# Kernel optimization log

Hardware: AMD Instinct MI355X
Metric: run time of the kernel (lower is better)

The kernel has to match this reference:

```python
import jax, jax.numpy as jnp
import numpy as np

B, S, SE = 4, 1024, 1024
E, H, M = 768, 12, 100
D = E // H
EPS = 1e-5
GELU_C = 0.7978845608028654  # sqrt(2/pi)


def _ln(x, g, b):
    mu = x.mean(-1, keepdims=True)
    v = ((x - mu) ** 2).mean(-1, keepdims=True)
    return g * (x - mu) / jnp.sqrt(v + EPS) + b


def _gelu(x):
    return 0.5 * x * (1.0 + jnp.tanh(GELU_C * (x + 0.044715 * x ** 3)))


def _split(x):  # [b,s,E] -> [b,H,s,D]
    b, s, _ = x.shape
    return x.reshape(b, s, H, D).transpose(0, 2, 1, 3)


def _merge(x):  # [b,H,s,D] -> [b,s,E]
    b, h, s, d = x.shape
    return x.transpose(0, 2, 1, 3).reshape(b, s, h * d)


def _forward(x, encoder_features, ln1_g, ln1_b, ln2_g, ln2_b,
             c_attn_w, c_attn_b, attn_proj_w, attn_proj_b,
             memory_features, mem_attn_w, mem_attn_b, mem_alpha_w, mem_alpha_b,
             fcq_w, fcq_b, fck_w, fck_b, fcv_w, fcv_b, enc_proj_w, enc_proj_b,
             fc_alpha1_w, fc_alpha1_b, fc_alpha2_w, fc_alpha2_b,
             mlp_fc_w, mlp_fc_b, mlp_proj_w, mlp_proj_b, mask_encoder):
    # ---- memory-augmented self-attention (note: original has NO 1/sqrt(d) scaling here) ----
    h = _ln(x, ln1_g, ln1_b)
    qkv = h @ c_attn_w + c_attn_b
    q, k, v = jnp.split(qkv, 3, axis=-1)
    q, k, v = _split(q), _split(k), _split(v)
    w = jax.nn.softmax(jnp.einsum('bhqd,bhkd->bhqk', q, k), axis=-1)
    a = _merge(jnp.einsum('bhqk,bhkd->bhqd', w, v))
    # memory slots are batch-independent -> compute once, broadcast over batch
    mem = memory_features[0] @ mem_attn_w + mem_attn_b  # [M, 2E]
    mk, mv = jnp.split(mem, 2, axis=-1)
    mk = mk.reshape(M, H, D).transpose(1, 2, 0)  # [H,D,M]
    mv = mv.reshape(M, H, D).transpose(1, 0, 2)  # [H,M,D]
    wm = jax.nn.softmax(jnp.einsum('bhqd,hdm->bhqm', q, mk), axis=-1)
    a1 = _merge(jnp.einsum('bhqm,hmd->bhqd', wm, mv))
    al = jax.nn.sigmoid(jnp.concatenate([a, a1], -1) @ mem_alpha_w + mem_alpha_b)
    a = al * a + (1.0 - al) * a1
    a = a @ attn_proj_w + attn_proj_b
    a = x + a  # residual (dropout = identity in eval)

    # ---- two cross-attentions sharing weights and ln_1 ----
    ha = _ln(a, ln1_g, ln1_b)

    def enc_dec(enc):
        qe = _split(ha @ fcq_w + fcq_b)
        ke = _split(enc @ fck_w + fck_b)
        ve = _split(enc @ fcv_w + fcv_b)
        we = jnp.einsum('bhqd,bhkd->bhqk', qe, ke) / np.float32(np.sqrt(D))
        we = jnp.where(mask_encoder, jnp.float32(-10000.0), we)
        we = jax.nn.softmax(we, axis=-1)
        o = _merge(jnp.einsum('bhqk,bhkd->bhqd', we, ve))
        return o @ enc_proj_w + enc_proj_b

    e1 = enc_dec(_ln(encoder_features[:, 0], ln1_g, ln1_b))
    e2 = enc_dec(_ln(encoder_features[:, 1], ln1_g, ln1_b))
    al1 = jax.nn.sigmoid(jnp.concatenate([a, e1], -1) @ fc_alpha1_w + fc_alpha1_b)
    al2 = jax.nn.sigmoid(jnp.concatenate([a, e2], -1) @ fc_alpha2_w + fc_alpha2_b)
    e1 = al1 * a + (1.0 - al1) * e1
    e2 = al2 * a + (1.0 - al2) * e2
    a = (e1 + e2) / np.float32(np.sqrt(2.0))

    # ---- MLP ----
    hm = _ln(a, ln2_g, ln2_b)
    m = _gelu(hm @ mlp_fc_w + mlp_fc_b) @ mlp_proj_w + mlp_proj_b
    return a + m


def setup_inputs() -> dict:
    key = jax.random.key(0)
    ks = iter(jax.random.split(key, 48))

    def rn(shape, s=0.02):
        return jax.random.normal(next(ks), shape, jnp.float32) * s

    return dict(
        x=jax.random.normal(next(ks), (B, S, E), jnp.float32),
        encoder_features=jax.random.normal(next(ks), (B, 2, SE, E), jnp.float32),
        mask_encoder=jax.random.bernoulli(next(ks), 0.1, (B, 1, 1, SE)),
        ln1_g=jnp.ones(E, jnp.float32), ln1_b=jnp.zeros(E, jnp.float32),
        ln2_g=jnp.ones(E, jnp.float32), ln2_b=jnp.zeros(E, jnp.float32),
        c_attn_w=rn((E, 3 * E)), c_attn_b=jnp.zeros(3 * E, jnp.float32),
        attn_proj_w=rn((E, E)), attn_proj_b=jnp.zeros(E, jnp.float32),
        memory_features=rn((1, M, E), 1.0),
        mem_attn_w=rn((E, 2 * E)), mem_attn_b=jnp.zeros(2 * E, jnp.float32),
        mem_alpha_w=rn((2 * E, E)), mem_alpha_b=jnp.zeros(E, jnp.float32),
        fcq_w=rn((E, E)), fcq_b=jnp.zeros(E, jnp.float32),
        fck_w=rn((E, E)), fck_b=jnp.zeros(E, jnp.float32),
        fcv_w=rn((E, E)), fcv_b=jnp.zeros(E, jnp.float32),
        enc_proj_w=rn((E, E)), enc_proj_b=jnp.zeros(E, jnp.float32),
        fc_alpha1_w=rn((2 * E, E)), fc_alpha1_b=jnp.zeros(E, jnp.float32),
        fc_alpha2_w=rn((2 * E, E)), fc_alpha2_b=jnp.zeros(E, jnp.float32),
        mlp_fc_w=rn((E, 4 * E)), mlp_fc_b=jnp.zeros(4 * E, jnp.float32),
        mlp_proj_w=rn((4 * E, E)), mlp_proj_b=jnp.zeros(E, jnp.float32),
    )


def reference(x, encoder_features, mask_encoder, ln1_g, ln1_b, ln2_g, ln2_b,
              c_attn_w, c_attn_b, attn_proj_w, attn_proj_b,
              memory_features, mem_attn_w, mem_attn_b, mem_alpha_w, mem_alpha_b,
              fcq_w, fcq_b, fck_w, fck_b, fcv_w, fcv_b, enc_proj_w, enc_proj_b,
              fc_alpha1_w, fc_alpha1_b, fc_alpha2_w, fc_alpha2_b,
              mlp_fc_w, mlp_fc_b, mlp_proj_w, mlp_proj_b):
    return _forward(x, encoder_features, ln1_g, ln1_b, ln2_g, ln2_b,
                    c_attn_w, c_attn_b, attn_proj_w, attn_proj_b,
                    memory_features, mem_attn_w, mem_attn_b, mem_alpha_w, mem_alpha_b,
                    fcq_w, fcq_b, fck_w, fck_b, fcv_w, fcv_b, enc_proj_w, enc_proj_b,
                    fc_alpha1_w, fc_alpha1_b, fc_alpha2_w, fc_alpha2_b,
                    mlp_fc_w, mlp_fc_b, mlp_proj_w, mlp_proj_b, mask_encoder)
```

## Files before the change

### kernel.cpp

```cpp
#include <hip/hip_runtime.h>

typedef __bf16 bf16_t;
typedef __bf16 bf16x8v __attribute__((ext_vector_type(8)));
typedef float f32x4 __attribute__((ext_vector_type(4)));

#define CB 4
#define CE 768
#define CH 12
#define CD 64

__device__ __forceinline__ float fexp2(float x) { return __builtin_amdgcn_exp2f(x); }

__device__ __forceinline__ void gload16(const void* g, void* l) {
    __builtin_amdgcn_global_load_lds((const __attribute__((address_space(1))) void*)g,
                                     (__attribute__((address_space(3))) void*)l, 16, 0, 0);
}

__device__ __forceinline__ void xcd_remap(int& bx, int& by, int gx, int gy) {
    int nwg = gx * gy;
    if ((nwg & 7) == 0) {
        int lin = by * gx + bx;
        int lin2 = (lin & 7) * (nwg >> 3) + (lin >> 3);
        bx = lin2 % gx;
        by = lin2 / gx;
    }
}

template<int BM, int BN, int CONCAT, int ACT, int RES, int OUT, int CMODE>
__global__ __launch_bounds__(256)
void gemm_n(const bf16_t* __restrict__ A0, const bf16_t* __restrict__ A1,
            const bf16_t* __restrict__ Bt, const float* __restrict__ bias,
            const float* __restrict__ bias2, const void* __restrict__ resid,
            void* __restrict__ C, void* __restrict__ C2, void* __restrict__ C3,
            int M, int N, int K, int lda, int ldc)
{
    constexpr int WM = BM / 2, WN = BN / 2, RM = WM / 16, RN = WN / 16;
    __shared__ __align__(16) bf16_t As0[BM * 64], As1[BM * 64];
    __shared__ __align__(16) bf16_t Bs0[BN * 64], Bs1[BN * 64];

    const int t = threadIdx.x;
    const int lane = t & 63, wave = t >> 6;
    int bx = blockIdx.x, by = blockIdx.y;
    xcd_remap(bx, by, gridDim.x, gridDim.y);
    const int m0 = by * BM, n0 = bx * BN;
    const int wm = (wave & 1) * WM, wn = (wave >> 1) * WN;
    const int fr = lane & 15, quad = lane >> 4;

    const int lr = lane >> 3;
    const int kof = ((lane & 7) ^ lr) * 8;

    const bf16_t* A1b = A1;
    if (CMODE == 6) A1b = A1 + (n0 >= 768 ? (long)4096 * 768 : 0);

    f32x4 acc[RM][RN];
#pragma unroll
    for (int i = 0; i < RM; i++)
#pragma unroll
        for (int j = 0; j < RN; j++)
#pragma unroll
            for (int p = 0; p < 4; p++) acc[i][j][p] = 0.f;

    auto stage = [&](bf16_t* As, bf16_t* Bs, int kt) {
        const bf16_t* Ab = A0;
        int kk = kt;
        if (CONCAT && kt >= 768) { Ab = A1b; kk = kt - 768; }
        const bf16_t* asrc = Ab + (long)(m0 + wave * 8 + lr) * lda + kk + kof;
#pragma unroll
        for (int c = 0; c < BM / 32; ++c)
            gload16(asrc + (long)c * 32 * lda, &As[(c * 32 + wave * 8) * 64]);
        const bf16_t* bsrc = Bt + (long)(n0 + wave * 8 + lr) * K + kt + kof;
#pragma unroll
        for (int c = 0; c < BN / 32; ++c)
            gload16(bsrc + (long)c * 32 * K, &Bs[(c * 32 + wave * 8) * 64]);
    };

    const int sw = fr & 7;
    auto compute = [&](const bf16_t* As, const bf16_t* Bs) {
        bf16x8v af[RM][2], bfr[RN][2];
        const int s0 = quad ^ sw;
#pragma unroll
        for (int i = 0; i < RM; ++i) {
            const char* rb = (const char*)As + (wm + i * 16 + fr) * 128;
            af[i][0] = *(const bf16x8v*)(rb + (s0 << 4));
            af[i][1] = *(const bf16x8v*)(rb + ((s0 ^ 4) << 4));
        }
#pragma unroll
        for (int j = 0; j < RN; ++j) {
            const char* rb = (const char*)Bs + (wn + j * 16 + fr) * 128;
            bfr[j][0] = *(const bf16x8v*)(rb + (s0 << 4));
            bfr[j][1] = *(const bf16x8v*)(rb + ((s0 ^ 4) << 4));
        }
#pragma unroll
        for (int ks = 0; ks < 2; ++ks)
#pragma unroll
            for (int i = 0; i < RM; ++i)
#pragma unroll
                for (int j = 0; j < RN; ++j)
                    acc[i][j] = __builtin_amdgcn_mfma_f32_16x16x32_bf16(af[i][ks], bfr[j][ks], acc[i][j], 0, 0, 0);
    };

    const int nk = K >> 6;
    stage(As0, Bs0, 0);
    __syncthreads();
    for (int kt = 0; kt + 2 <= nk; kt += 2) {
        stage(As1, Bs1, (kt + 1) << 6);
        compute(As0, Bs0);
        __syncthreads();
        if (kt + 2 < nk) stage(As0, Bs0, (kt + 2) << 6);
        compute(As1, Bs1);
        __syncthreads();
    }

    const int rq = quad * 4, cn = fr;
#pragma unroll
    for (int i = 0; i < RM; i++)
#pragma unroll
        for (int j = 0; j < RN; j++) {
            int col = n0 + wn + j * 16 + cn;
            int t3 = (CMODE == 4 || CMODE == 5) ? (col / 768) : 0;
            int cc = col - t3 * 768;
            float bv = 0.f;
            if (CMODE == 5)      bv = t3 ? bias2[cc] : bias[cc];
            else if (CMODE == 6) bv = (col < 768) ? bias[col] : bias2[col - 768];
            else if (bias)       bv = bias[col];
            const int row0 = m0 + wm + i * 16 + rq;
            float vv[4];
#pragma unroll
            for (int p = 0; p < 4; p++) {
                float v = acc[i][j][p] + bv;
                if (ACT == 1) v = 1.f / (1.f + __expf(-v));
                if (ACT == 2) {
                    float u2 = 1.5957691216057308f * (v + 0.044715f * v * v * v);
                    v = v / (1.f + __expf(-u2));
                }
                if (RES == 2) v += ((const float*)resid)[(long)(row0 + p) * ldc + col];
                vv[p] = v;
            }
            if (CMODE == 0) {
#pragma unroll
                for (int p = 0; p < 4; p++) {
                    long idx = (long)(row0 + p) * ldc + col;
                    if (OUT == 0)      ((bf16_t*)C)[idx] = (bf16_t)vv[p];
                    else if (OUT == 1) ((float*)C)[idx] = vv[p];
                    else { ((float*)C)[idx] = vv[p]; ((bf16_t*)C2)[idx] = (bf16_t)vv[p]; }
                }
            } else if (CMODE == 6) {
                long base = (col < 768) ? 0 : ((long)4096 * 768 - 768);
#pragma unroll
                for (int p = 0; p < 4; p++)
                    ((bf16_t*)C)[base + (long)(row0 + p) * 768 + col] = (bf16_t)vv[p];
            } else if (CMODE == 7) {
#pragma unroll
                for (int p = 0; p < 4; p++) {
                    long idx = (long)(row0 + p) * ldc + col;
                    float a  = (float)((const bf16_t*)C2)[idx];
                    float a1 = (float)((const bf16_t*)C3)[idx];
                    ((bf16_t*)C)[idx] = (bf16_t)(vv[p] * a + (1.f - vv[p]) * a1);
                }
            } else {
                int bb = row0 >> 10, ss0 = row0 & 1023;
                int hh = cc >> 6, dd = cc & 63;
                long srow = (long)(bb * CH + hh) * 1024 + ss0;
                long tbase = (((long)(bb * CH + hh) * 64) + dd) * 1024 + ss0;
                union { ushort4 u4; bf16_t b[4]; } pk;
#pragma unroll
                for (int p = 0; p < 4; p++) pk.b[p] = (bf16_t)vv[p];
                if (CMODE == 2) {
#pragma unroll
                    for (int p = 0; p < 4; p++)
                        ((bf16_t*)C)[(srow + p) * 64 + dd] = pk.b[p];
                } else if (CMODE == 5) {
                    if (t3 == 0) {
#pragma unroll
                        for (int p = 0; p < 4; p++)
                            ((bf16_t*)C)[(srow + p) * 64 + dd] = pk.b[p];
                    } else {
                        *(ushort4*)((bf16_t*)C2 + tbase) = pk.u4;
                    }
                } else {
                    if (t3 == 0) {
#pragma unroll
                        for (int p = 0; p < 4; p++)
                            ((bf16_t*)C)[(srow + p) * 64 + dd] = pk.b[p];
                    } else if (t3 == 1) {
#pragma unroll
                        for (int p = 0; p < 4; p++)
                            ((bf16_t*)C2)[(srow + p) * 64 + dd] = pk.b[p];
                    } else {
                        *(ushort4*)((bf16_t*)C3 + tbase) = pk.u4;
                    }
                }
            }
        }
}

template<int MODE, int QR>
__global__ __launch_bounds__(256)
void flash_attn(const bf16_t* __restrict__ Q, const bf16_t* __restrict__ K,
                const bf16_t* __restrict__ V, const int* __restrict__ mask,
                bf16_t* __restrict__ O)
{
    constexpr int QG = QR / 64;
    __shared__ __align__(16) bf16_t Qs[QR * 64];
    __shared__ __align__(16) bf16_t Ks0[64 * 64], Ks1[64 * 64];
    __shared__ __align__(16) bf16_t Vs[64 * 64];

    const int t = threadIdx.x;
    const int lane = t & 63, wave = t >> 6;
    int bx = blockIdx.x, bz = blockIdx.z;
    {
        int nwg = gridDim.x * gridDim.z;
        if ((nwg & 7) == 0) {
            int lin = bz * gridDim.x + bx;
            int lin2 = (lin & 7) * (nwg >> 3) + (lin >> 3);
            bx = lin2 % gridDim.x;
            bz = lin2 / gridDim.x;
        }
    }
    const int zq = (MODE == 1) ? (bz % 48) : bz;
    const int b = zq / CH, h = bz % CH;
    const long eoff = (MODE == 1) ? (long)(bz / 48) * ((long)4096 * 768) : 0;
    const int q0 = bx * QR;

    const bf16_t* Qb = Q + (long)zq * 65536 + (long)q0 * 64;
    const bf16_t* Kb = (MODE == 2) ? K + (long)h * (128 * 64) : K + (long)bz * 65536;
    const bf16_t* Vb = (MODE == 2) ? V + (long)h * (64 * 128) : V + (long)bz * 65536;
    const int ldv = (MODE == 2) ? 128 : 1024;
    const int NT = (MODE == 2) ? 2 : 16;
    constexpr float SCL = (MODE == 1) ? 0.18033688011112042f : 1.4426950408889634f;

    const int lr = lane >> 3, kof = ((lane & 7) ^ lr) * 8;

    auto stageK = [&](bf16_t* Ks, int kt) {
#pragma unroll
        for (int c = 0; c < 2; ++c) {
            int r = wave * 8 + c * 32;
            gload16(Kb + (long)(kt * 64 + r + lr) * 64 + kof, &Ks[r * 64]);
        }
    };
    auto stageV = [&](int kt) {
#pragma unroll
        for (int c = 0; c < 2; ++c) {
            int r = wave * 8 + c * 32;
            gload16(Vb + (long)(r + lr) * ldv + kt * 64 + kof, &Vs[r * 64]);
        }
    };

    stageK(Ks0, 0);
#pragma unroll
    for (int c = 0; c < QR / 32; ++c) {
        int r = wave * 8 + c * 32;
        gload16(Qb + (long)(r + lr) * 64 + kof, &Qs[r * 64]);
    }
    __syncthreads();

    const int fr = lane & 15, quad = lane >> 4;
    const int sw = fr & 7;
    bf16x8v qf[QG][2];
#pragma unroll
    for (int g = 0; g < QG; g++)
#pragma unroll
        for (int ks = 0; ks < 2; ks++) {
            const char* rb = (const char*)Qs + (wave * (16 * QG) + g * 16 + fr) * 128;
            bf16x8v raw = *(const bf16x8v*)(rb + (((quad ^ sw) ^ (ks << 2)) << 4));
#pragma unroll
            for (int i = 0; i < 8; i++) qf[g][ks][i] = (bf16_t)((float)raw[i] * SCL);
        }

    bf16_t* Ps = &Qs[wave * (16 * QG) * 64];

    f32x4 o[4][QG];
    float mrow[QG], lrow[QG];
#pragma unroll
    for (int g = 0; g < QG; g++) { mrow[g] = -1e30f; lrow[g] = 0.f; }
#pragma unroll
    for (int j = 0; j < 4; j++)
#pragma unroll
        for (int g = 0; g < QG; g++)
#pragma unroll
            for (int p = 0; p < 4; p++) o[j][g][p] = 0.f;

    auto qkt_sm = [&](const bf16_t* Ks, int kt) {
        f32x4 s[4][QG];
#pragma unroll
        for (int j = 0; j < 4; j++)
#pragma unroll
            for (int g = 0; g < QG; g++)
#pragma unroll
                for (int p = 0; p < 4; p++) s[j][g][p] = 0.f;
        __builtin_amdgcn_s_setprio(1);
#pragma unroll
        for (int ks = 0; ks < 2; ks++) {
            bf16x8v bk[4];
#pragma unroll
            for (int j = 0; j < 4; j++) {
                const char* rb = (const char*)Ks + (j * 16 + fr) * 128;
                bk[j] = *(const bf16x8v*)(rb + (((quad ^ sw) ^ (ks << 2)) << 4));
            }
#pragma unroll
            for (int j = 0; j < 4; j++)
#pragma unroll
                for (int g = 0; g < QG; g++)
                    s[j][g] = __builtin_amdgcn_mfma_f32_16x16x32_bf16(bk[j], qf[g][ks], s[j][g], 0, 0, 0);
        }
        __builtin_amdgcn_s_setprio(0);
        if (MODE == 1) {
#pragma unroll
            for (int j = 0; j < 4; j++) {
                int4 mv = *(const int4*)&mask[(long)b * 1024 + kt * 64 + j * 16 + quad * 4];
#pragma unroll
                for (int g = 0; g < QG; g++) {
                    s[j][g][0] = mv.x ? -14426.95f : s[j][g][0];
                    s[j][g][1] = mv.y ? -14426.95f : s[j][g][1];
                    s[j][g][2] = mv.z ? -14426.95f : s[j][g][2];
                    s[j][g][3] = mv.w ? -14426.95f : s[j][g][3];
                }
            }
        }
        if (MODE == 2) {
#pragma unroll
            for (int j = 0; j < 4; j++)
#pragma unroll
                for (int p = 0; p < 4; p++)
                    if (kt * 64 + j * 16 + quad * 4 + p >= 100)
#pragma unroll
                        for (int g = 0; g < QG; g++) s[j][g][p] = -1e30f;
        }
        float tmax[QG];
        bool need = false;
#pragma unroll
        for (int g = 0; g < QG; g++) {
            float tm = s[0][g][0];
#pragma unroll
            for (int j = 0; j < 4; j++)
#pragma unroll
                for (int p = 0; p < 4; p++) tm = fmaxf(tm, s[j][g][p]);
            tm = fmaxf(tm, __shfl_xor(tm, 16, 64));
            tm = fmaxf(tm, __shfl_xor(tm, 32, 64));
            tmax[g] = tm;
            need = need || (tm > mrow[g] + 8.f);
        }
        if (__any(need ? 1 : 0)) {
#pragma unroll
            for (int g = 0; g < QG; g++) {
                float mnew = fmaxf(mrow[g], tmax[g]);
                float alpha = fexp2(mrow[g] - mnew);
                lrow[g] *= alpha;
                mrow[g] = mnew;
                float arow[4];
#pragma unroll
                for (int p = 0; p < 4; p++)
                    arow[p] = __shfl(alpha, (lane & 48) | (quad * 4 + p), 64);
#pragma unroll
                for (int j = 0; j < 4; j++)
#pragma unroll
                    for (int p = 0; p < 4; p++) o[j][g][p] *= arow[p];
            }
        }
#pragma unroll
        for (int g = 0; g < QG; g++) {
            float rs = 0.f;
#pragma unroll
            for (int j = 0; j < 4; j++)
#pragma unroll
                for (int p = 0; p < 4; p++) {
                    float e = fexp2(s[j][g][p] - mrow[g]);
                    s[j][g][p] = e;
                    rs += e;
                }
            rs += __shfl_xor(rs, 16, 64);
            rs += __shfl_xor(rs, 32, 64);
            lrow[g] += rs;
        }
#pragma unroll
        for (int j = 0; j < 4; j++)
#pragma unroll
            for (int g = 0; g < QG; g++) {
                union { uint2 u; bf16_t bb[4]; } pk;
#pragma unroll
                for (int p = 0; p < 4; p++) pk.bb[p] = (bf16_t)s[j][g][p];
                int row = g * 16 + fr;
                *(uint2*)((char*)Ps + row * 128 +
                          (((j * 2 + (quad >> 1)) ^ sw) << 4) + ((quad & 1) << 3)) = pk.u;
            }
    };

    auto pv = [&]() {
        __builtin_amdgcn_s_setprio(1);
#pragma unroll
        for (int ks = 0; ks < 2; ks++) {
            bf16x8v af[QG], bv[4];
#pragma unroll
            for (int g = 0; g < QG; g++) {
                const char* rb = (const char*)Ps + (g * 16 + fr) * 128;
                af[g] = *(const bf16x8v*)(rb + (((quad ^ sw) ^ (ks << 2)) << 4));
            }
#pragma unroll
            for (int j = 0; j < 4; j++) {
                const char* rb = (const char*)Vs + (j * 16 + fr) * 128;
                bv[j] = *(const bf16x8v*)(rb + (((quad ^ sw) ^ (ks << 2)) << 4));
            }
#pragma unroll
            for (int j = 0; j < 4; j++)
#pragma unroll
                for (int g = 0; g < QG; g++)
                    o[j][g] = __builtin_amdgcn_mfma_f32_16x16x32_bf16(af[g], bv[j], o[j][g], 0, 0, 0);
        }
        __builtin_amdgcn_s_setprio(0);
    };

    for (int kt = 0; kt < NT; kt += 2) {
        stageV(kt);
        if (kt + 1 < NT) stageK(Ks1, kt + 1);
        qkt_sm(Ks0, kt);
        __syncthreads();
        pv();
        __syncthreads();
        stageV(kt + 1);
        if (kt + 2 < NT) stageK(Ks0, kt + 2);
        qkt_sm(Ks1, kt + 1);
        __syncthreads();
        pv();
        __syncthreads();
    }
#pragma unroll
    for (int g = 0; g < QG; g++) {
        float linv[4];
#pragma unroll
        for (int p = 0; p < 4; p++)
            linv[p] = 1.f / __shfl(lrow[g], (lane & 48) | (quad * 4 + p), 64);
#pragma unroll
        for (int p = 0; p < 4; p++) {
            int srow = q0 + wave * (16 * QG) + g * 16 + quad * 4 + p;
            long base = ((long)b * 1024 + srow) * 768 + h * 64 + eoff;
#pragma unroll
            for (int j = 0; j < 4; j++)
                O[base + j * 16 + fr] = (bf16_t)(o[j][g][p] * linv[p]);
        }
    }
}

__device__ __forceinline__ void ln_body(const float* in, bf16_t* out,
                                        const float* g, const float* b,
                                        long base, long ob, int t)
{
    __shared__ float red[4];
    float v0 = in[base + t], v1 = in[base + t + 256], v2 = in[base + t + 512];
    float s = v0 + v1 + v2;
    for (int m = 32; m; m >>= 1) s += __shfl_xor(s, m, 64);
    if ((t & 63) == 0) red[t >> 6] = s;
    __syncthreads();
    s = red[0] + red[1] + red[2] + red[3];
    __syncthreads();
    const float mu = s * (1.f / 768.f);
    float d0 = v0 - mu, d1 = v1 - mu, d2 = v2 - mu;
    float q = d0 * d0 + d1 * d1 + d2 * d2;
    for (int m = 32; m; m >>= 1) q += __shfl_xor(q, m, 64);
    if ((t & 63) == 0) red[t >> 6] = q;
    __syncthreads();
    q = red[0] + red[1] + red[2] + red[3];
    const float rstd = rsqrtf(q * (1.f / 768.f) + 1e-5f);
    out[ob + t]       = (bf16_t)(g[t]       * d0 * rstd + b[t]);
    out[ob + t + 256] = (bf16_t)(g[t + 256] * d1 * rstd + b[t + 256]);
    out[ob + t + 512] = (bf16_t)(g[t + 512] * d2 * rstd + b[t + 512]);
}

__global__ __launch_bounds__(256)
void ln_kernel(const float* __restrict__ in, bf16_t* __restrict__ out,
               const float* __restrict__ g, const float* __restrict__ b)
{
    const int r = blockIdx.x;
    ln_body(in, out, g, b, (long)r * CE, (long)r * CE, threadIdx.x);
}

__global__ __launch_bounds__(256)
void ln_enc(const float* __restrict__ encf, bf16_t* __restrict__ out,
            const float* __restrict__ g, const float* __restrict__ b)
{
    const int r = blockIdx.x;
    const int e = r >> 12, rr = r & 4095, bb = rr >> 10, s = rr & 1023;
    ln_body(encf, out, g, b, ((long)(bb * 2 + e) * 1024 + s) * CE, (long)r * CE, threadIdx.x);
}

__global__ void fuse_gates2(const bf16_t* __restrict__ gal, const bf16_t* __restrict__ eo,
                            float* __restrict__ rf)
{
    const long SZel = (long)4096 * 768;
    long idx = (long)blockIdx.x * 256 + threadIdx.x;
    float g1 = (float)gal[idx], g2 = (float)gal[idx + SZel];
    float e1 = (float)eo[idx],  e2 = (float)eo[idx + SZel];
    float r = rf[idx];
    float v = g1 * r + (1.f - g1) * e1 + g2 * r + (1.f - g2) * e2;
    rf[idx] = v * 0.7071067811865476f;
}

__global__ void zero_out(float* __restrict__ out)
{
    out[blockIdx.x * 256 + threadIdx.x] = 0.f;
}

#define NTW 12
struct TTab {
    const float* src[NTW];
    unsigned long dst[NTW];
    int kn[NTW];
    int pre[NTW + 1];
};

__global__ void transpose_all(TTab tt, char* __restrict__ ws)
{
    __shared__ bf16_t tile[32][33];
    int tb = blockIdx.x;
    int e = 0;
#pragma unroll
    for (int i = 0; i < NTW; i++) if (tb >= tt.pre[i + 1]) e = i + 1;
    int local = tb - tt.pre[e];
    const int K = tt.kn[e] >> 16, N = tt.kn[e] & 0xffff;
    const float* in = tt.src[e];
    bf16_t* out = (bf16_t*)(ws + tt.dst[e]);
    const int ntx = N / 32;
    const int n0 = (local % ntx) * 32, k0 = (local / ntx) * 32;
    int tx = threadIdx.x, ty = threadIdx.y;
    for (int i = ty; i < 32; i += 8)
        tile[i][tx] = (bf16_t)in[(long)(k0 + i) * N + n0 + tx];
    __syncthreads();
    for (int i = ty; i < 32; i += 8)
        out[(long)(n0 + i) * K + k0 + tx] = tile[tx][i];
}

__global__ void cast_pad_mem(const float* __restrict__ memf, bf16_t* __restrict__ out)
{
    int idx = blockIdx.x * 256 + threadIdx.x;
    int row = idx / 768;
    out[idx] = (row < 100) ? (bf16_t)memf[idx] : (bf16_t)0.f;
}

__global__ void repack_mem(const bf16_t* __restrict__ mem, bf16_t* __restrict__ mkt,
                           bf16_t* __restrict__ mvt)
{
    int idx = blockIdx.x * 256 + threadIdx.x;
    int d = idx & 63;
    int slot = (idx >> 6) & 127;
    int h = idx >> 13;
    bf16_t kv = (slot < 100) ? mem[slot * 1536 + h * CD + d] : (bf16_t)0.f;
    bf16_t vv = (slot < 100) ? mem[slot * 1536 + CE + h * CD + d] : (bf16_t)0.f;
    mkt[idx] = kv;
    mvt[((long)h * 64 + d) * 128 + slot] = vv;
}

extern "C" void kernel_launch(void* const* d_in, const int* in_sizes, int n_in,
                              void* d_out, int out_size, void* d_ws, size_t ws_size,
                              hipStream_t stream)
{
    (void)in_sizes; (void)n_in; (void)out_size;
    const float* x        = (const float*)d_in[0];
    const float* encf     = (const float*)d_in[1];
    const int*   maskenc  = (const int*)d_in[2];
    const float* ln1_g    = (const float*)d_in[3];
    const float* ln1_b    = (const float*)d_in[4];
    const float* ln2_g    = (const float*)d_in[5];
    const float* ln2_b    = (const float*)d_in[6];
    const float* c_attn_w = (const float*)d_in[7];
    const float* c_attn_b = (const float*)d_in[8];
    const float* aproj_w  = (const float*)d_in[9];
    const float* aproj_b  = (const float*)d_in[10];
    const float* memf     = (const float*)d_in[11];
    const float* mattn_w  = (const float*)d_in[12];
    const float* mattn_b  = (const float*)d_in[13];
    const float* malpha_w = (const float*)d_in[14];
    const float* malpha_b = (const float*)d_in[15];
    const float* fcq_w    = (const float*)d_in[16];
    const float* fcq_b    = (const float*)d_in[17];
    const float* fck_w    = (const float*)d_in[18];
    const float* fck_b    = (const float*)d_in[19];
    const float* fcv_w    = (const float*)d_in[20];
    const float* fcv_b    = (const float*)d_in[21];
    const float* eproj_w  = (const float*)d_in[22];
    const float* eproj_b  = (const float*)d_in[23];
    const float* fa1_w    = (const float*)d_in[24];
    const float* fa1_b    = (const float*)d_in[25];
    const float* fa2_w    = (const float*)d_in[26];
    const float* fa2_b    = (const float*)d_in[27];
    const float* mfc_w    = (const float*)d_in[28];
    const float* mfc_b    = (const float*)d_in[29];
    const float* mproj_w  = (const float*)d_in[30];
    const float* mproj_b  = (const float*)d_in[31];
    float* dout = (float*)d_out;

    size_t off = 0;
    auto alloc = [&](size_t bytes) -> void* {
        void* p = (char*)d_ws + off;
        off = (off + bytes + 255) & ~(size_t)255;
        return p;
    };
    const size_t SZ = (size_t)4096 * 768 * 2;
    const long SZel = (long)4096 * 768;
    bf16_t* wt_cattn  = (bf16_t*)alloc((size_t)2304 * 768 * 2);
    bf16_t* wt_aproj  = (bf16_t*)alloc((size_t)768 * 768 * 2);
    bf16_t* wt_malpha = (bf16_t*)alloc((size_t)768 * 1536 * 2);
    bf16_t* wt_fcq    = (bf16_t*)alloc((size_t)768 * 768 * 2);
    bf16_t* wt_fck    = (bf16_t*)alloc((size_t)768 * 768 * 2);
    bf16_t* wt_fcv    = (bf16_t*)alloc((size_t)768 * 768 * 2);
    bf16_t* wt_eproj  = (bf16_t*)alloc((size_t)768 * 768 * 2);
    bf16_t* wt_fa1    = (bf16_t*)alloc((size_t)768 * 1536 * 2);
    bf16_t* wt_fa2    = (bf16_t*)alloc((size_t)768 * 1536 * 2);
    bf16_t* wt_mfc    = (bf16_t*)alloc((size_t)3072 * 768 * 2);
    bf16_t* wt_mproj  = (bf16_t*)alloc((size_t)768 * 3072 * 2);
    bf16_t* wt_mattn  = (bf16_t*)alloc((size_t)1536 * 768 * 2);
    bf16_t* memb   = (bf16_t*)alloc((size_t)128 * 768 * 2);
    bf16_t* membuf = (bf16_t*)alloc((size_t)128 * 1536 * 2);
    bf16_t* mkt    = (bf16_t*)alloc((size_t)CH * 128 * 64 * 2);
    bf16_t* mvt    = (bf16_t*)alloc((size_t)CH * 64 * 128 * 2);
    bf16_t* bufA   = (bf16_t*)alloc(SZ);
    bf16_t* qbuf   = (bf16_t*)alloc(SZ);
    bf16_t* kbuf   = (bf16_t*)alloc(2 * SZ);
    bf16_t* vtbuf  = (bf16_t*)alloc(2 * SZ);
    bf16_t* asbuf  = (bf16_t*)alloc(2 * SZ);
    bf16_t* bufB   = (bf16_t*)alloc(2 * SZ);
    float*  residf = (float*)alloc((size_t)4096 * 768 * 4);
    bf16_t* residb = (bf16_t*)alloc(SZ);

    if (off > ws_size) {
        zero_out<<<12288, 256, 0, stream>>>(dout);
        return;
    }
    bf16_t* mid = kbuf;
    bf16_t* galbuf = kbuf;
    bf16_t* eobuf = bufB;

    const dim3 blk(256);

    TTab tt;
    {
        const float* srcs[NTW] = {c_attn_w, aproj_w, malpha_w, fcq_w, fck_w, fcv_w,
                                  eproj_w, fa1_w, fa2_w, mfc_w, mproj_w, mattn_w};
        bf16_t* dsts[NTW] = {wt_cattn, wt_aproj, wt_malpha, wt_fcq, wt_fck, wt_fcv,
                             wt_eproj, wt_fa1, wt_fa2, wt_mfc, wt_mproj, wt_mattn};
        int Ks[NTW] = {768, 768, 1536, 768, 768, 768, 768, 1536, 1536, 768, 3072, 768};
        int Ns[NTW] = {2304, 768, 768, 768, 768, 768, 768, 768, 768, 3072, 768, 1536};
        int acc = 0;
        for (int i = 0; i < NTW; i++) {
            tt.src[i] = srcs[i];
            tt.dst[i] = (unsigned long)((char*)dsts[i] - (char*)d_ws);
            tt.kn[i] = (Ks[i] << 16) | Ns[i];
            tt.pre[i] = acc;
            acc += (Ks[i] / 32) * (Ns[i] / 32);
        }
        tt.pre[NTW] = acc;
        transpose_all<<<acc, dim3(32, 8), 0, stream>>>(tt, (char*)d_ws);
    }

    cast_pad_mem<<<384, blk, 0, stream>>>(memf, memb);
    gemm_n<64,64,0,0,0,0,0><<<dim3(24, 2), blk, 0, stream>>>(
        memb, nullptr, wt_mattn, mattn_b, nullptr, nullptr, membuf, nullptr, nullptr,
        128, 1536, 768, 768, 1536);
    repack_mem<<<384, blk, 0, stream>>>(membuf, mkt, mvt);

    ln_kernel<<<4096, blk, 0, stream>>>(x, bufA, ln1_g, ln1_b);
    gemm_n<128,64,0,0,0,0,4><<<dim3(36, 32), blk, 0, stream>>>(
        bufA, nullptr, wt_cattn, c_attn_b, nullptr, nullptr, qbuf, kbuf, vtbuf,
        4096, 2304, 768, 768, 0);

    flash_attn<0,64><<<dim3(16, 1, 48), blk, 0, stream>>>(qbuf, kbuf, vtbuf, nullptr, asbuf);
    flash_attn<2,64><<<dim3(16, 1, 48), blk, 0, stream>>>(qbuf, mkt, mvt, nullptr, asbuf + SZel);

    gemm_n<64,64,1,1,0,0,7><<<dim3(12, 64), blk, 0, stream>>>(
        asbuf, asbuf + SZel, wt_malpha, malpha_b, nullptr, nullptr, bufA, asbuf, asbuf + SZel,
        4096, 768, 1536, 768, 768);
    gemm_n<64,64,0,0,2,2,0><<<dim3(12, 64), blk, 0, stream>>>(
        bufA, nullptr, wt_aproj, aproj_b, nullptr, x, residf, residb, nullptr,
        4096, 768, 768, 768, 768);

    ln_kernel<<<4096, blk, 0, stream>>>(residf, bufA, ln1_g, ln1_b);
    gemm_n<64,64,0,0,0,0,2><<<dim3(12, 64), blk, 0, stream>>>(
        bufA, nullptr, wt_fcq, fcq_b, nullptr, nullptr, qbuf, nullptr, nullptr,
        4096, 768, 768, 768, 0);

    ln_enc<<<8192, blk, 0, stream>>>(encf, bufB, ln1_g, ln1_b);
    gemm_n<128,64,0,0,0,0,5><<<dim3(24, 64), blk, 0, stream>>>(
        bufB, nullptr, wt_fck, fck_b, fcv_b, nullptr, kbuf, vtbuf, nullptr,
        8192, 1536, 768, 768, 0);
    flash_attn<1,128><<<dim3(8, 1, 96), blk, 0, stream>>>(
        qbuf, kbuf, vtbuf, maskenc, asbuf);
    gemm_n<128,64,0,0,0,0,0><<<dim3(12, 64), blk, 0, stream>>>(
        asbuf, nullptr, wt_eproj, eproj_b, nullptr, nullptr, eobuf, nullptr, nullptr,
        8192, 768, 768, 768, 768);
    gemm_n<128,64,1,1,0,0,6><<<dim3(24, 32), blk, 0, stream>>>(
        residb, eobuf, wt_fa1, fa1_b, fa2_b, nullptr, galbuf, nullptr, nullptr,
        4096, 1536, 1536, 768, 768);
    fuse_gates2<<<12288, blk, 0, stream>>>(galbuf, eobuf, residf);

    ln_kernel<<<4096, blk, 0, stream>>>(residf, bufA, ln2_g, ln2_b);
    gemm_n<128,64,0,2,0,0,0><<<dim3(48, 32), blk, 0, stream>>>(
        bufA, nullptr, wt_mfc, mfc_b, nullptr, nullptr, mid, nullptr, nullptr,
        4096, 3072, 768, 768, 3072);
    gemm_n<128,64,0,0,2,1,0><<<dim3(12, 32), blk, 0, stream>>>(
        mid, nullptr, wt_mproj, mproj_b, nullptr, residf, dout, nullptr, nullptr,
        4096, 768, 3072, 3072, 768);
}
```

Baseline: 541.1 us.

## Fuse memory-slot prep, merge self/memory attention launches, fuse gates with LayerNorm

Several fusions land at once. The memory cast is folded into the weight-transpose launch, and the memory GEMM epilogue writes the repacked K/V layouts directly, which removes the cast_pad_mem and repack_mem kernels and the intermediate buffer. Self-attention and memory attention now run in one flash_attn launch with a doubled grid. The row-sum shuffle reduction moves out of the inner loop to the end, and the gate combine is fused with the second LayerNorm. Together these cut launch count and memory round-trips, at the cost of more branching inside the kernels.

```diff
diff --git a/kernel.cpp b/kernel.cpp
--- a/kernel.cpp
+++ b/kernel.cpp
@@ -117,7 +117,7 @@
 #pragma unroll
         for (int j = 0; j < RN; j++) {
             int col = n0 + wn + j * 16 + cn;
-            int t3 = (CMODE == 4 || CMODE == 5) ? (col / 768) : 0;
+            int t3 = (CMODE == 4 || CMODE == 5 || CMODE == 9) ? (col / 768) : 0;
             int cc = col - t3 * 768;
             float bv = 0.f;
             if (CMODE == 5)      bv = t3 ? bias2[cc] : bias[cc];
@@ -157,6 +157,20 @@
                     float a1 = (float)((const bf16_t*)C3)[idx];
                     ((bf16_t*)C)[idx] = (bf16_t)(vv[p] * a + (1.f - vv[p]) * a1);
                 }
+            } else if (CMODE == 9) {
+                int hh = cc >> 6, dd = cc & 63;
+                if (t3 == 0) {
+#pragma unroll
+                    for (int p = 0; p < 4; p++)
+                        ((bf16_t*)C)[(long)hh * 8192 + (row0 + p) * 64 + dd] =
+                            (row0 + p < 100) ? (bf16_t)vv[p] : (bf16_t)0.f;
+                } else {
+                    union { ushort4 u4; bf16_t b[4]; } pk;
+#pragma unroll
+                    for (int p = 0; p < 4; p++)
+                        pk.b[p] = (row0 + p < 100) ? (bf16_t)vv[p] : (bf16_t)0.f;
+                    *(ushort4*)((bf16_t*)C2 + (long)hh * 8192 + dd * 128 + row0) = pk.u4;
+                }
             } else {
                 int bb = row0 >> 10, ss0 = row0 & 1023;
                 int hh = cc >> 6, dd = cc & 63;
@@ -197,7 +211,8 @@
 template<int MODE, int QR>
 __global__ __launch_bounds__(256)
 void flash_attn(const bf16_t* __restrict__ Q, const bf16_t* __restrict__ K,
-                const bf16_t* __restrict__ V, const int* __restrict__ mask,
+                const bf16_t* __restrict__ V, const bf16_t* __restrict__ K2,
+                const bf16_t* __restrict__ V2, const int* __restrict__ mask,
                 bf16_t* __restrict__ O)
 {
     constexpr int QG = QR / 64;
@@ -217,16 +232,18 @@
             bz = lin2 / gridDim.x;
         }
     }
-    const int zq = (MODE == 1) ? (bz % 48) : bz;
-    const int b = zq / CH, h = bz % CH;
-    const long eoff = (MODE == 1) ? (long)(bz / 48) * ((long)4096 * 768) : 0;
+    const bool memrole = (MODE == 3) && (bz >= 48);
+    const int zq = (MODE == 1) ? (bz % 48) : (memrole ? bz - 48 : bz);
+    const int b = zq / CH, h = zq % CH;
+    long obase = (MODE == 1) ? (long)(bz / 48) * ((long)4096 * 768)
+                             : (memrole ? (long)4096 * 768 : 0);
     const int q0 = bx * QR;
 
     const bf16_t* Qb = Q + (long)zq * 65536 + (long)q0 * 64;
-    const bf16_t* Kb = (MODE == 2) ? K + (long)h * (128 * 64) : K + (long)bz * 65536;
-    const bf16_t* Vb = (MODE == 2) ? V + (long)h * (64 * 128) : V + (long)bz * 65536;
-    const int ldv = (MODE == 2) ? 128 : 1024;
-    const int NT = (MODE == 2) ? 2 : 16;
+    const bf16_t* Kb = memrole ? K2 + (long)h * 8192 : K + (long)bz * 65536;
+    const bf16_t* Vb = memrole ? V2 + (long)h * 8192 : V + (long)bz * 65536;
+    const int ldv = memrole ? 128 : 1024;
+    const int NT = memrole ? 2 : 16;
     constexpr float SCL = (MODE == 1) ? 0.18033688011112042f : 1.4426950408889634f;
 
     const int lr = lane >> 3, kof = ((lane & 7) ^ lr) * 8;
@@ -317,7 +334,7 @@
                 }
             }
         }
-        if (MODE == 2) {
+        if (MODE == 3 && memrole) {
 #pragma unroll
             for (int j = 0; j < 4; j++)
 #pragma unroll
@@ -368,8 +385,6 @@
                     s[j][g][p] = e;
                     rs += e;
                 }
-            rs += __shfl_xor(rs, 16, 64);
-            rs += __shfl_xor(rs, 32, 64);
             lrow[g] += rs;
         }
 #pragma unroll
@@ -425,6 +440,8 @@
     }
 #pragma unroll
     for (int g = 0; g < QG; g++) {
+        lrow[g] += __shfl_xor(lrow[g], 16, 64);
+        lrow[g] += __shfl_xor(lrow[g], 32, 64);
         float linv[4];
 #pragma unroll
         for (int p = 0; p < 4; p++)
@@ -432,7 +449,7 @@
 #pragma unroll
         for (int p = 0; p < 4; p++) {
             int srow = q0 + wave * (16 * QG) + g * 16 + quad * 4 + p;
-            long base = ((long)b * 1024 + srow) * 768 + h * 64 + eoff;
+            long base = ((long)b * 1024 + srow) * 768 + h * 64 + obase;
 #pragma unroll
             for (int j = 0; j < 4; j++)
                 O[base + j * 16 + fr] = (bf16_t)(o[j][g][p] * linv[p]);
@@ -440,12 +457,11 @@
     }
 }
 
-__device__ __forceinline__ void ln_body(const float* in, bf16_t* out,
+__device__ __forceinline__ void ln_vals(float v0, float v1, float v2, bf16_t* out,
                                         const float* g, const float* b,
-                                        long base, long ob, int t)
+                                        long ob, int t)
 {
     __shared__ float red[4];
-    float v0 = in[base + t], v1 = in[base + t + 256], v2 = in[base + t + 512];
     float s = v0 + v1 + v2;
     for (int m = 32; m; m >>= 1) s += __shfl_xor(s, m, 64);
     if ((t & 63) == 0) red[t >> 6] = s;
@@ -470,7 +486,10 @@
                const float* __restrict__ g, const float* __restrict__ b)
 {
     const int r = blockIdx.x;
-    ln_body(in, out, g, b, (long)r * CE, (long)r * CE, threadIdx.x);
+    const int t = threadIdx.x;
+    long base = (long)r * CE;
+    ln_vals(in[base + t], in[base + t + 256], in[base + t + 512],
+            out, g, b, base, t);
 }
 
 __global__ __launch_bounds__(256)
@@ -478,20 +497,34 @@
             const float* __restrict__ g, const float* __restrict__ b)
 {
     const int r = blockIdx.x;
+    const int t = threadIdx.x;
     const int e = r >> 12, rr = r & 4095, bb = rr >> 10, s = rr & 1023;
-    ln_body(encf, out, g, b, ((long)(bb * 2 + e) * 1024 + s) * CE, (long)r * CE, threadIdx.x);
-}
-
-__global__ void fuse_gates2(const bf16_t* __restrict__ gal, const bf16_t* __restrict__ eo,
-                            float* __restrict__ rf)
+    long base = ((long)(bb * 2 + e) * 1024 + s) * CE;
+    ln_vals(encf[base + t], encf[base + t + 256], encf[base + t + 512],
+            out, g, b, (long)r * CE, t);
+}
+
+__global__ __launch_bounds__(256)
+void fuse_gates_ln(const bf16_t* __restrict__ gal, const bf16_t* __restrict__ eo,
+                   float* __restrict__ rf, bf16_t* __restrict__ out,
+                   const float* __restrict__ g, const float* __restrict__ b)
 {
     const long SZel = (long)4096 * 768;
-    long idx = (long)blockIdx.x * 256 + threadIdx.x;
-    float g1 = (float)gal[idx], g2 = (float)gal[idx + SZel];
-    float e1 = (float)eo[idx],  e2 = (float)eo[idx + SZel];
-    float r = rf[idx];
-    float v = g1 * r + (1.f - g1) * e1 + g2 * r + (1.f - g2) * e2;
-    rf[idx] = v * 0.7071067811865476f;
+    const int r = blockIdx.x, t = threadIdx.x;
+    long base = (long)r * CE;
+    float v[3];
+#pragma unroll
+    for (int k = 0; k < 3; k++) {
+        long idx = base + t + k * 256;
+        float g1 = (float)gal[idx], g2 = (float)gal[idx + SZel];
+        float e1 = (float)eo[idx],  e2 = (float)eo[idx + SZel];
+        float rr = rf[idx];
+        float vv = (g1 * rr + (1.f - g1) * e1 + g2 * rr + (1.f - g2) * e2)
+                   * 0.7071067811865476f;
+        rf[idx] = vv;
+        v[k] = vv;
+    }
+    ln_vals(v[0], v[1], v[2], out, g, b, base, t);
 }
 
 __global__ void zero_out(float* __restrict__ out)
@@ -505,12 +538,21 @@
     unsigned long dst[NTW];
     int kn[NTW];
     int pre[NTW + 1];
+    const float* memf;
+    unsigned long membOff;
 };
 
 __global__ void transpose_all(TTab tt, char* __restrict__ ws)
 {
     __shared__ bf16_t tile[32][33];
     int tb = blockIdx.x;
+    if (tb >= tt.pre[NTW]) {
+        int idx = (tb - tt.pre[NTW]) * 256 + threadIdx.y * 32 + threadIdx.x;
+        int row = idx / 768;
+        ((bf16_t*)(ws + tt.membOff))[idx] =
+            (row < 100) ? (bf16_t)tt.memf[idx] : (bf16_t)0.f;
+        return;
+    }
     int e = 0;
 #pragma unroll
     for (int i = 0; i < NTW; i++) if (tb >= tt.pre[i + 1]) e = i + 1;
@@ -526,26 +568,6 @@
     __syncthreads();
     for (int i = ty; i < 32; i += 8)
         out[(long)(n0 + i) * K + k0 + tx] = tile[tx][i];
-}
-
-__global__ void cast_pad_mem(const float* __restrict__ memf, bf16_t* __restrict__ out)
-{
-    int idx = blockIdx.x * 256 + threadIdx.x;
-    int row = idx / 768;
-    out[idx] = (row < 100) ? (bf16_t)memf[idx] : (bf16_t)0.f;
-}
-
-__global__ void repack_mem(const bf16_t* __restrict__ mem, bf16_t* __restrict__ mkt,
-                           bf16_t* __restrict__ mvt)
-{
-    int idx = blockIdx.x * 256 + threadIdx.x;
-    int d = idx & 63;
-    int slot = (idx >> 6) & 127;
-    int h = idx >> 13;
-    bf16_t kv = (slot < 100) ? mem[slot * 1536 + h * CD + d] : (bf16_t)0.f;
-    bf16_t vv = (slot < 100) ? mem[slot * 1536 + CE + h * CD + d] : (bf16_t)0.f;
-    mkt[idx] = kv;
-    mvt[((long)h * 64 + d) * 128 + slot] = vv;
 }
 
 extern "C" void kernel_launch(void* const* d_in, const int* in_sizes, int n_in,
@@ -608,7 +630,6 @@
     bf16_t* wt_mproj  = (bf16_t*)alloc((size_t)768 * 3072 * 2);
     bf16_t* wt_mattn  = (bf16_t*)alloc((size_t)1536 * 768 * 2);
     bf16_t* memb   = (bf16_t*)alloc((size_t)128 * 768 * 2);
-    bf16_t* membuf = (bf16_t*)alloc((size_t)128 * 1536 * 2);
     bf16_t* mkt    = (bf16_t*)alloc((size_t)CH * 128 * 64 * 2);
     bf16_t* mvt    = (bf16_t*)alloc((size_t)CH * 64 * 128 * 2);
     bf16_t* bufA   = (bf16_t*)alloc(SZ);
@@ -647,22 +668,22 @@
             acc += (Ks[i] / 32) * (Ns[i] / 32);
         }
         tt.pre[NTW] = acc;
-        transpose_all<<<acc, dim3(32, 8), 0, stream>>>(tt, (char*)d_ws);
-    }
-
-    cast_pad_mem<<<384, blk, 0, stream>>>(memf, memb);
-    gemm_n<64,64,0,0,0,0,0><<<dim3(24, 2), blk, 0, stream>>>(
-        memb, nullptr, wt_mattn, mattn_b, nullptr, nullptr, membuf, nullptr, nullptr,
+        tt.memf = memf;
+        tt.membOff = (unsigned long)((char*)memb - (char*)d_ws);
+        transpose_all<<<acc + 384, dim3(32, 8), 0, stream>>>(tt, (char*)d_ws);
+    }
+
+    gemm_n<64,64,0,0,0,0,9><<<dim3(24, 2), blk, 0, stream>>>(
+        memb, nullptr, wt_mattn, mattn_b, nullptr, nullptr, mkt, mvt, nullptr,
         128, 1536, 768, 768, 1536);
-    repack_mem<<<384, blk, 0, stream>>>(membuf, mkt, mvt);
 
     ln_kernel<<<4096, blk, 0, stream>>>(x, bufA, ln1_g, ln1_b);
     gemm_n<128,64,0,0,0,0,4><<<dim3(36, 32), blk, 0, stream>>>(
         bufA, nullptr, wt_cattn, c_attn_b, nullptr, nullptr, qbuf, kbuf, vtbuf,
         4096, 2304, 768, 768, 0);
 
-    flash_attn<0,64><<<dim3(16, 1, 48), blk, 0, stream>>>(qbuf, kbuf, vtbuf, nullptr, asbuf);
-    flash_attn<2,64><<<dim3(16, 1, 48), blk, 0, stream>>>(qbuf, mkt, mvt, nullptr, asbuf + SZel);
+    flash_attn<3,64><<<dim3(16, 1, 96), blk, 0, stream>>>(
+        qbuf, kbuf, vtbuf, mkt, mvt, nullptr, asbuf);
 
     gemm_n<64,64,1,1,0,0,7><<<dim3(12, 64), blk, 0, stream>>>(
         asbuf, asbuf + SZel, wt_malpha, malpha_b, nullptr, nullptr, bufA, asbuf, asbuf + SZel,
@@ -681,16 +702,15 @@
         bufB, nullptr, wt_fck, fck_b, fcv_b, nullptr, kbuf, vtbuf, nullptr,
         8192, 1536, 768, 768, 0);
     flash_attn<1,128><<<dim3(8, 1, 96), blk, 0, stream>>>(
-        qbuf, kbuf, vtbuf, maskenc, asbuf);
+        qbuf, kbuf, vtbuf, nullptr, nullptr, maskenc, asbuf);
     gemm_n<128,64,0,0,0,0,0><<<dim3(12, 64), blk, 0, stream>>>(
         asbuf, nullptr, wt_eproj, eproj_b, nullptr, nullptr, eobuf, nullptr, nullptr,
         8192, 768, 768, 768, 768);
     gemm_n<128,64,1,1,0,0,6><<<dim3(24, 32), blk, 0, stream>>>(
         residb, eobuf, wt_fa1, fa1_b, fa2_b, nullptr, galbuf, nullptr, nullptr,
         4096, 1536, 1536, 768, 768);
-    fuse_gates2<<<12288, blk, 0, stream>>>(galbuf, eobuf, residf);
-
-    ln_kernel<<<4096, blk, 0, stream>>>(residf, bufA, ln2_g, ln2_b);
+    fuse_gates_ln<<<4096, blk, 0, stream>>>(galbuf, eobuf, residf, bufA, ln2_g, ln2_b);
+
     gemm_n<128,64,0,2,0,0,0><<<dim3(48, 32), blk, 0, stream>>>(
         bufA, nullptr, wt_mfc, mfc_b, nullptr, nullptr, mid, nullptr, nullptr,
         4096, 3072, 768, 768, 3072);
```

Measured after the change: 536.1 us. No clear change (-0.9%).
